# Kernel optimization log

Measured on AMD Instinct MI355X. Metric: run time of the kernel, lower is better.

## Reference

```python
import jax, jax.numpy as jnp
import numpy as np

NUM_ATOMS = 100
D = 32        # initial_atom_dim
H = 16        # hidden_dim (multiplicity per irrep)
NB = 16       # edge_dim / number of bessel basis functions
CUT = 6.0     # radius_cutoff
DEG = 4.0     # degree_norm
OUT = 1       # output_dim
INV4PI = 1.0 / np.sqrt(4.0 * np.pi)  # 'integral' SH normalization


def _bessel(d, nb, cut):
    # e3nn soft_one_hot_linspace(basis='bessel', cutoff=True) * sqrt(nb)
    x = d[:, None]
    n = jnp.arange(1, nb + 1, dtype=d.dtype)
    safe = jnp.maximum(x, 1e-9)
    out = np.sqrt(2.0 / cut) * jnp.sin(n * jnp.pi * x / cut) / safe
    return out * (x < cut) * np.sqrt(float(nb))


def _fc(x, w1, w2):
    # e3nn FullyConnectedNet: fan-in normalized linear layers, silu, no bias
    h = jax.nn.silu(x @ w1 / np.sqrt(x.shape[-1]))
    return h @ w2 / np.sqrt(w1.shape[-1])


def _forward(atomic_numbers, edge_index, coords, atom_emb,
             fc0_w1, fc0_w2, fc1_w1, fc1_w2, w_readout):
    src, dst = edge_index[0], edge_index[1]
    N = coords.shape[0]
    E = src.shape[0]

    vec = coords[src] - coords[dst]                      # [E,3]
    dist = jnp.linalg.norm(vec, axis=-1)                 # [E]
    unit = vec / jnp.maximum(dist, 1e-9)[:, None]

    # spherical harmonics, l=0 and l=1, 'integral' normalization
    y0 = jnp.full((E,), INV4PI, dtype=coords.dtype)      # [E]
    y1 = (np.sqrt(3.0) * INV4PI) * unit                  # [E,3]
    basis = _bessel(dist, NB, CUT)                       # [E,NB]

    x = atom_emb[atomic_numbers]                         # [N,D] (row 0 is padding)

    # ---- layer 0: scalars (D x0e) x (1x0e+1x1o) -> H x0e + H x1o ----
    w = _fc(basis, fc0_w1, fc0_w2)                       # [E, 2*D*H] per-edge TP weights
    wa = w[:, : D * H].reshape(E, D, H)
    wb = w[:, D * H:].reshape(E, D, H)
    xs = x[src]
    n0 = 1.0 / np.sqrt(D)                                # path fan-in norm
    m0 = jnp.einsum('ed,edh->eh', xs, wa) * y0[:, None] * n0          # [E,H]
    m1 = jnp.einsum('ed,edh->eh', xs, wb)[:, :, None] * y1[:, None, :] * n0  # [E,H,3]
    z0 = jax.ops.segment_sum(m0, dst, num_segments=N) / DEG           # [N,H]
    z1 = jax.ops.segment_sum(m1, dst, num_segments=N) / DEG           # [N,H,3]

    # ---- layer 1: (H x0e + H x1o) x (1x0e+1x1o) -> same irreps, skip-connected ----
    w = _fc(basis, fc1_w1, fc1_w2)                       # [E, 4*H*H]
    w1_ = w[:, 0 * H * H:1 * H * H].reshape(E, H, H)     # 0e x 0e -> 0e
    w2_ = w[:, 1 * H * H:2 * H * H].reshape(E, H, H)     # 0e x 1o -> 1o
    w3_ = w[:, 2 * H * H:3 * H * H].reshape(E, H, H)     # 1o x 0e -> 1o
    w4_ = w[:, 3 * H * H:4 * H * H].reshape(E, H, H)     # 1o x 1o -> 0e (CG = dot/sqrt(3))
    s, v = z0[src], z1[src]
    n1 = 1.0 / np.sqrt(2 * H)                            # two paths per output irrep
    dot = jnp.einsum('ehm,em->eh', v, y1) / np.sqrt(3.0)
    o0 = (jnp.einsum('eh,ehk->ek', s, w1_) * y0[:, None]
          + jnp.einsum('eh,ehk->ek', dot, w4_)) * n1
    o1 = (jnp.einsum('eh,ehk->ek', s, w2_)[:, :, None] * y1[:, None, :]
          + jnp.einsum('ehm,ehk->ekm', v, w3_) * y0[:, None, None]) * n1
    z0 = jax.ops.segment_sum(o0, dst, num_segments=N) / DEG + z0      # skip
    z1 = jax.ops.segment_sum(o1, dst, num_segments=N) / DEG + z1

    # ---- scalar readout (o3.Linear onto 0e) + graph sum-pool ----
    node_scalar = z0 @ w_readout / np.sqrt(H)            # [N,OUT]
    return jnp.sum(node_scalar, axis=0)                  # [OUT]


def setup_inputs() -> dict:
    key = jax.random.key(0)
    ks = jax.random.split(key, 9)
    N, E = 10000, 160000
    atomic_numbers = jax.random.randint(ks[0], (N,), 0, NUM_ATOMS)
    coords = jax.random.normal(ks[1], (N, 3), dtype=jnp.float32)
    edge_index = jax.random.randint(ks[2], (2, E), 0, N)
    atom_emb = jax.random.normal(ks[3], (NUM_ATOMS, D), dtype=jnp.float32).at[0].set(0.0)
    fc0_w1 = jax.random.normal(ks[4], (NB, H), dtype=jnp.float32)
    fc0_w2 = jax.random.normal(ks[5], (H, 2 * D * H), dtype=jnp.float32)
    fc1_w1 = jax.random.normal(ks[6], (NB, H), dtype=jnp.float32)
    fc1_w2 = jax.random.normal(ks[7], (H, 4 * H * H), dtype=jnp.float32)
    w_readout = jax.random.normal(ks[8], (H, OUT), dtype=jnp.float32)
    return {"atomic_numbers": atomic_numbers, "coords": coords, "edge_index": edge_index,
            "atom_emb": atom_emb, "fc0_w1": fc0_w1, "fc0_w2": fc0_w2,
            "fc1_w1": fc1_w1, "fc1_w2": fc1_w2, "w_readout": w_readout}


def reference(atomic_numbers, coords, edge_index, atom_emb,
              fc0_w1, fc0_w2, fc1_w1, fc1_w2, w_readout):
    return _forward(atomic_numbers, edge_index, coords, atom_emb,
                    fc0_w1, fc0_w2, fc1_w1, fc1_w2, w_readout)
```

## Files before the change

kernel.cpp:

```cpp
#include <hip/hip_runtime.h>
#include <math.h>


namespace {
constexpr int   NATOMS   = 100;
constexpr int   CAP      = 64;
constexpr float PI_F     = 3.14159265358979323846f;
constexpr float INV4PI_F = 0.28209479177387814f;
constexpr float SQRT3_F  = 1.7320508075688772f;
constexpr float CUT_F    = 6.0f;
constexpr float BASIS_C  = 2.3094010767585034f;
constexpr float N0_F     = 0.17677669529663687f;
constexpr float K0_F = INV4PI_F * N0_F * 0.0625f;
constexpr float K1_F = SQRT3_F * INV4PI_F * N0_F * 0.0625f;
constexpr float P2SC = INV4PI_F * N0_F * (1.0f / 64.0f);
}

__device__ __forceinline__ float silu_fast(float x) {
  return x / (1.0f + __expf(-x));
}

__device__ __forceinline__ float block_reduce_sum(float v) {
  #pragma unroll
  for (int o = 32; o > 0; o >>= 1) v += __shfl_down(v, o, 64);
  __shared__ float ls[8];
  int lane = threadIdx.x & 63;
  int w    = threadIdx.x >> 6;
  if (lane == 0) ls[w] = v;
  __syncthreads();
  float s = 0.f;
  if (threadIdx.x == 0) {
    int nw = (blockDim.x + 63) >> 6;
    for (int i = 0; i < nw; ++i) s += ls[i];
  }
  return s;
}

__global__ void table_kernel(const float* __restrict__ atom_emb,
                             const float* __restrict__ fc0_w2,
                             const float* __restrict__ fc1_w2,
                             const float* __restrict__ w_readout,
                             float* __restrict__ TI,
                             float* __restrict__ G1T, float* __restrict__ G4T,
                             int* __restrict__ dcur,
                             float* __restrict__ out,
                             int N2) {
  int b = blockIdx.x;
  int tt = threadIdx.x;
  if (b < NATOMS) {
    int j = tt >> 4;
    int h = tt & 15;
    float s0 = 0.f, s1 = 0.f;
    #pragma unroll
    for (int d = 0; d < 32; ++d) {
      float x = atom_emb[b * 32 + d];
      s0 = fmaf(x, fc0_w2[j * 1024 + d * 16 + h], s0);
      s1 = fmaf(x, fc0_w2[j * 1024 + 512 + d * 16 + h], s1);
    }
    TI[b * 512 + j * 32 + 2 * h]     = s0;
    TI[b * 512 + j * 32 + 2 * h + 1] = s1;
  } else if (b == NATOMS) {
    int j = tt >> 4;
    int h = tt & 15;
    float g1 = 0.f, g4 = 0.f;
    #pragma unroll
    for (int k = 0; k < 16; ++k) {
      float r = w_readout[k];
      g1 = fmaf(fc1_w2[j * 1024 + h * 16 + k], r, g1);
      g4 = fmaf(fc1_w2[j * 1024 + 768 + h * 16 + k], r, g4);
    }
    G1T[h * 16 + j] = g1;
    G4T[h * 16 + j] = g4;
    if (tt == 0) *out = 0.f;
  } else {
    int idx = (b - NATOMS - 1) * 256 + tt;
    if (idx < N2) dcur[idx] = 0;
  }
}

__global__ void __launch_bounds__(256)
edge_kernel(const int* __restrict__ ei,
            const float* __restrict__ coords,
            const int* __restrict__ an,
            const float* __restrict__ TI,
            const float* __restrict__ fc0_w1,
            const float* __restrict__ fc1_w1,
            int* __restrict__ dcur, int* __restrict__ scur,
            float2* __restrict__ mbuf,
            float4* __restrict__ ubuf,
            float4* __restrict__ sbuf,
            float* __restrict__ hbuf,
            int E) {
  int lane = threadIdx.x & 63;
  int g    = threadIdx.x >> 4;
  int t    = threadIdx.x & 15;
  int base = lane & 48;

  float w0c[16], w1c[16];
  #pragma unroll
  for (int k = 0; k < 16; ++k) {
    w0c[k] = fc0_w1[k * 16 + t];
    w1c[k] = fc1_w1[k * 16 + t];
  }

  const float angc = PI_F / CUT_F;
  int eA = blockIdx.x * 32 + g;
  int eB = eA + 16;
  bool vA = eA < E, vB = eB < E;
  int eAc = vA ? eA : 0, eBc = vB ? eB : 0;

  int sA = ei[eAc], dA = ei[E + eAc];
  int sB = ei[eBc], dB = ei[E + eBc];
  float sxA = coords[3 * sA + 0], syA = coords[3 * sA + 1], szA = coords[3 * sA + 2];
  float dxA = coords[3 * dA + 0], dyA = coords[3 * dA + 1], dzA = coords[3 * dA + 2];
  float sxB = coords[3 * sB + 0], syB = coords[3 * sB + 1], szB = coords[3 * sB + 2];
  float dxB = coords[3 * dB + 0], dyB = coords[3 * dB + 1], dzB = coords[3 * dB + 2];
  int aA = an[sA], aB = an[sB];

  float vxA = sxA - dxA, vyA = syA - dyA, vzA = szA - dzA;
  float vxB = sxB - dxB, vyB = syB - dyB, vzB = szB - dzB;
  float distA = sqrtf(vxA * vxA + vyA * vyA + vzA * vzA);
  float distB = sqrtf(vxB * vxB + vyB * vyB + vzB * vzB);
  float ivA = 1.0f / fmaxf(distA, 1e-9f);
  float ivB = 1.0f / fmaxf(distB, 1e-9f);
  float uxA = vxA * ivA, uyA = vyA * ivA, uzA = vzA * ivA;
  float uxB = vxB * ivB, uyB = vyB * ivB, uzB = vzB * ivB;
  float bcA = (distA < CUT_F) ? (BASIS_C * ivA) : 0.0f;
  float bcB = (distB < CUT_F) ? (BASIS_C * ivB) : 0.0f;

  int dsAv = 0, ssAv = 0, dsBv = 0, ssBv = 0;
  if (t == 0) {
    if (vA) {
      int p = atomicAdd(&dcur[dA], 1), q = atomicAdd(&scur[sA], 1);
      dsAv = dA * CAP + min(p, CAP - 1);
      ssAv = sA * CAP + min(q, CAP - 1);
      ubuf[dsAv] = make_float4(uxA, uyA, uzA, distA);
      sbuf[ssAv] = make_float4(uxA, uyA, uzA, distA);
    }
    if (vB) {
      int p = atomicAdd(&dcur[dB], 1), q = atomicAdd(&scur[sB], 1);
      dsBv = dB * CAP + min(p, CAP - 1);
      ssBv = sB * CAP + min(q, CAP - 1);
      ubuf[dsBv] = make_float4(uxB, uyB, uzB, distB);
      sbuf[ssBv] = make_float4(uxB, uyB, uzB, distB);
    }
  }

  float angA = angc * distA, angB = angc * distB;
  float scA = __sinf(angA), twA = 2.0f * __cosf(angA), spA = 0.f;
  float scB = __sinf(angB), twB = 2.0f * __cosf(angB), spB = 0.f;
  float a0A = 0.f, a1A = 0.f, a0B = 0.f, a1B = 0.f;
  #pragma unroll
  for (int k = 0; k < 16; ++k) {
    a0A = fmaf(scA, w0c[k], a0A);
    a1A = fmaf(scA, w1c[k], a1A);
    a0B = fmaf(scB, w0c[k], a0B);
    a1B = fmaf(scB, w1c[k], a1B);
    float snA = fmaf(twA, scA, -spA); spA = scA; scA = snA;
    float snB = fmaf(twB, scB, -spB); spB = scB; scB = snB;
  }
  float h0A = silu_fast(a0A * bcA * 0.25f);
  float h1A = silu_fast(a1A * bcA * 0.25f);
  float h0B = silu_fast(a0B * bcB * 0.25f);
  float h1B = silu_fast(a1B * bcB * 0.25f);

  int dsA = __shfl(dsAv, base, 64);
  int ssA = __shfl(ssAv, base, 64);
  int dsB = __shfl(dsBv, base, 64);
  int ssB = __shfl(ssBv, base, 64);

  const float2* tpA = (const float2*)(TI + aA * 512) + t;
  const float2* tpB = (const float2*)(TI + aB * 512) + t;
  float u0A = 0.f, u1A = 0.f, u0B = 0.f, u1B = 0.f;
  #pragma unroll
  for (int j = 0; j < 16; ++j) {
    float hjA = __shfl(h0A, base + j, 64);
    float hjB = __shfl(h0B, base + j, 64);
    float2 TA = tpA[j * 16];
    float2 TB = tpB[j * 16];
    u0A = fmaf(hjA, TA.x, u0A);
    u1A = fmaf(hjA, TA.y, u1A);
    u0B = fmaf(hjB, TB.x, u0B);
    u1B = fmaf(hjB, TB.y, u1B);
  }

  if (vA) {
    hbuf[(size_t)ssA * 16 + t] = h1A;
    mbuf[(size_t)dsA * 16 + t] = make_float2(K0_F * u0A, K1_F * u1A);
  }
  if (vB) {
    hbuf[(size_t)ssB * 16 + t] = h1B;
    mbuf[(size_t)dsB * 16 + t] = make_float2(K0_F * u0B, K1_F * u1B);
  }
}

__global__ void __launch_bounds__(256, 4)
node_kernel(const int* __restrict__ dcur,
            const int* __restrict__ scur,
            const float2* __restrict__ mbuf,
            const float4* __restrict__ ubuf,
            const float4* __restrict__ sbuf,
            const float* __restrict__ hbuf,
            const float* __restrict__ G1T,
            const float* __restrict__ G4T,
            const float* __restrict__ w_readout,
            float* __restrict__ out,
            int N) {
  __shared__ float ggs[512];
  ggs[threadIdx.x]       = G1T[threadIdx.x];
  ggs[256 + threadIdx.x] = G4T[threadIdx.x];
  __syncthreads();

  int wave = threadIdx.x >> 6;
  int lane = threadIdx.x & 63;
  int g    = lane >> 4;
  int t    = lane & 15;
  int base = lane & 48;
  int node = blockIdx.x * 4 + wave;
  bool valid = node < N;

  float rr = w_readout[t];
  int cin  = valid ? min(dcur[node], CAP) : 0;
  int cout = valid ? min(scur[node], CAP) : 0;
  size_t nb = (size_t)(valid ? node : 0) * CAP;

  float a0 = 0.f, ax = 0.f, ay = 0.f, az = 0.f;
  for (int i = g; i < cin; i += 4) {
    float2 f  = mbuf[(nb + i) * 16 + t];
    float4 uu = ubuf[nb + i];
    a0 += f.x;
    ax = fmaf(f.y, uu.x, ax);
    ay = fmaf(f.y, uu.y, ay);
    az = fmaf(f.y, uu.z, az);
  }
  a0 += __shfl_xor(a0, 16, 64); a0 += __shfl_xor(a0, 32, 64);
  ax += __shfl_xor(ax, 16, 64); ax += __shfl_xor(ax, 32, 64);
  ay += __shfl_xor(ay, 16, 64); ay += __shfl_xor(ay, 32, 64);
  az += __shfl_xor(az, 16, 64); az += __shfl_xor(az, 32, 64);

  float srcv = (g == 0) ? a0 : ((g == 1) ? ax : (g == 2) ? ay : az);
  int tofs = (g == 0) ? 0 : 256;
  float o = 0.f;
  #pragma unroll
  for (int h = 0; h < 16; ++h) {
    float vh = __shfl(srcv, base + h, 64);
    o = fmaf(ggs[tofs + h * 16 + t], vh, o);
  }
  float Qt  = __shfl(o, t, 64);
  float Pxt = __shfl(o, 16 + t, 64);
  float Pyt = __shfl(o, 32 + t, 64);
  float Pzt = __shfl(o, 48 + t, 64);

  float c = 0.f;
  for (int i = g; i < cout; i += 4) {
    float h1 = hbuf[(nb + i) * 16 + t];
    float4 uu = sbuf[nb + i];
    c = fmaf(h1, fmaf(Pxt, uu.x, fmaf(Pyt, uu.y, fmaf(Pzt, uu.z, Qt))), c);
  }
  c *= P2SC;
  if (valid && g == 0) c = fmaf(a0 * rr, 0.25f, c);
  if (!valid) c = 0.f;

  float tot = block_reduce_sum(c);
  if (threadIdx.x == 0) atomicAdd(out, tot);
}

extern "C" void kernel_launch(void* const* d_in, const int* in_sizes, int n_in,
                              void* d_out, int out_size, void* d_ws, size_t ws_size,
                              hipStream_t stream) {
  const int*   an        = (const int*)d_in[0];
  const float* coords    = (const float*)d_in[1];
  const int*   ei        = (const int*)d_in[2];
  const float* atom_emb  = (const float*)d_in[3];
  const float* fc0_w1    = (const float*)d_in[4];
  const float* fc0_w2    = (const float*)d_in[5];
  const float* fc1_w1    = (const float*)d_in[6];
  const float* fc1_w2    = (const float*)d_in[7];
  const float* w_readout = (const float*)d_in[8];

  int N = in_sizes[0];
  int E = in_sizes[2] / 2;
  size_t slots = (size_t)N * CAP;

  float4* ubuf = (float4*)d_ws;
  float4* sbuf = ubuf + slots;
  float2* mbuf = (float2*)(sbuf + slots);
  float*  hbuf = (float*)(mbuf + slots * 16);
  float*  TI   = hbuf + slots * 16;
  float*  G1T  = TI + NATOMS * 512;
  float*  G4T  = G1T + 256;
  int*    dcur = (int*)(G4T + 256);
  int*    scur = dcur + N;
  float*  out = (float*)d_out;

  int blk = 256;
  int zgrid = (2 * N + blk - 1) / blk;
  table_kernel<<<NATOMS + 1 + zgrid, blk, 0, stream>>>(
      atom_emb, fc0_w2, fc1_w2, w_readout, TI, G1T, G4T, dcur, out, 2 * N);

  edge_kernel<<<(E + 31) / 32, blk, 0, stream>>>(
      ei, coords, an, TI, fc0_w1, fc1_w1, dcur, scur,
      mbuf, ubuf, sbuf, hbuf, E);

  node_kernel<<<(N + 3) / 4, blk, 0, stream>>>(
      dcur, scur, mbuf, ubuf, sbuf, hbuf, G1T, G4T, w_readout, out, N);
}
```

Before: 149.1 us.

## Replace source-bucketed edge buffers with per-node Z table and edge-parallel pass

Removes the second atomic bucketing by source node, along with the sbuf and hbuf slot buffers. The node kernel now writes per-node coefficient vectors (Q, Px, Py, Pz) to zbuf. A new edge-parallel kernel recomputes the layer-1 radial hidden h1 from a compact per-edge unit/dist record and gathers zbuf by source node. This is meant to cut atomics and the large scattered writes of 16 floats per edge, at the cost of an extra kernel launch, per-edge recomputation of the Bessel/MLP, and a random gather.

```diff
diff --git a/kernel.cpp b/kernel.cpp
--- a/kernel.cpp
+++ b/kernel.cpp
@@ -44,7 +44,7 @@
                              float* __restrict__ G1T, float* __restrict__ G4T,
                              int* __restrict__ dcur,
                              float* __restrict__ out,
-                             int N2) {
+                             int N) {
   int b = blockIdx.x;
   int tt = threadIdx.x;
   if (b < NATOMS) {
@@ -74,7 +74,7 @@
     if (tt == 0) *out = 0.f;
   } else {
     int idx = (b - NATOMS - 1) * 256 + tt;
-    if (idx < N2) dcur[idx] = 0;
+    if (idx < N) dcur[idx] = 0;
   }
 }
 
@@ -84,24 +84,19 @@
             const int* __restrict__ an,
             const float* __restrict__ TI,
             const float* __restrict__ fc0_w1,
-            const float* __restrict__ fc1_w1,
-            int* __restrict__ dcur, int* __restrict__ scur,
+            int* __restrict__ dcur,
             float2* __restrict__ mbuf,
             float4* __restrict__ ubuf,
-            float4* __restrict__ sbuf,
-            float* __restrict__ hbuf,
+            float4* __restrict__ evec,
             int E) {
   int lane = threadIdx.x & 63;
   int g    = threadIdx.x >> 4;
   int t    = threadIdx.x & 15;
   int base = lane & 48;
 
-  float w0c[16], w1c[16];
-  #pragma unroll
-  for (int k = 0; k < 16; ++k) {
-    w0c[k] = fc0_w1[k * 16 + t];
-    w1c[k] = fc1_w1[k * 16 + t];
-  }
+  float w0c[16];
+  #pragma unroll
+  for (int k = 0; k < 16; ++k) w0c[k] = fc0_w1[k * 16 + t];
 
   const float angc = PI_F / CUT_F;
   int eA = blockIdx.x * 32 + g;
@@ -128,46 +123,40 @@
   float bcA = (distA < CUT_F) ? (BASIS_C * ivA) : 0.0f;
   float bcB = (distB < CUT_F) ? (BASIS_C * ivB) : 0.0f;
 
-  int dsAv = 0, ssAv = 0, dsBv = 0, ssBv = 0;
+  int dsAv = 0, dsBv = 0;
   if (t == 0) {
     if (vA) {
-      int p = atomicAdd(&dcur[dA], 1), q = atomicAdd(&scur[sA], 1);
+      float4 rec = make_float4(uxA, uyA, uzA, distA);
+      int p = atomicAdd(&dcur[dA], 1);
       dsAv = dA * CAP + min(p, CAP - 1);
-      ssAv = sA * CAP + min(q, CAP - 1);
-      ubuf[dsAv] = make_float4(uxA, uyA, uzA, distA);
-      sbuf[ssAv] = make_float4(uxA, uyA, uzA, distA);
+      ubuf[dsAv] = rec;
+      evec[eA] = rec;
     }
     if (vB) {
-      int p = atomicAdd(&dcur[dB], 1), q = atomicAdd(&scur[sB], 1);
+      float4 rec = make_float4(uxB, uyB, uzB, distB);
+      int p = atomicAdd(&dcur[dB], 1);
       dsBv = dB * CAP + min(p, CAP - 1);
-      ssBv = sB * CAP + min(q, CAP - 1);
-      ubuf[dsBv] = make_float4(uxB, uyB, uzB, distB);
-      sbuf[ssBv] = make_float4(uxB, uyB, uzB, distB);
+      ubuf[dsBv] = rec;
+      evec[eB] = rec;
     }
   }
 
   float angA = angc * distA, angB = angc * distB;
   float scA = __sinf(angA), twA = 2.0f * __cosf(angA), spA = 0.f;
   float scB = __sinf(angB), twB = 2.0f * __cosf(angB), spB = 0.f;
-  float a0A = 0.f, a1A = 0.f, a0B = 0.f, a1B = 0.f;
+  float a0A = 0.f, a0B = 0.f;
   #pragma unroll
   for (int k = 0; k < 16; ++k) {
     a0A = fmaf(scA, w0c[k], a0A);
-    a1A = fmaf(scA, w1c[k], a1A);
     a0B = fmaf(scB, w0c[k], a0B);
-    a1B = fmaf(scB, w1c[k], a1B);
     float snA = fmaf(twA, scA, -spA); spA = scA; scA = snA;
     float snB = fmaf(twB, scB, -spB); spB = scB; scB = snB;
   }
   float h0A = silu_fast(a0A * bcA * 0.25f);
-  float h1A = silu_fast(a1A * bcA * 0.25f);
   float h0B = silu_fast(a0B * bcB * 0.25f);
-  float h1B = silu_fast(a1B * bcB * 0.25f);
 
   int dsA = __shfl(dsAv, base, 64);
-  int ssA = __shfl(ssAv, base, 64);
   int dsB = __shfl(dsBv, base, 64);
-  int ssB = __shfl(ssBv, base, 64);
 
   const float2* tpA = (const float2*)(TI + aA * 512) + t;
   const float2* tpB = (const float2*)(TI + aB * 512) + t;
@@ -184,26 +173,18 @@
     u1B = fmaf(hjB, TB.y, u1B);
   }
 
-  if (vA) {
-    hbuf[(size_t)ssA * 16 + t] = h1A;
-    mbuf[(size_t)dsA * 16 + t] = make_float2(K0_F * u0A, K1_F * u1A);
-  }
-  if (vB) {
-    hbuf[(size_t)ssB * 16 + t] = h1B;
-    mbuf[(size_t)dsB * 16 + t] = make_float2(K0_F * u0B, K1_F * u1B);
-  }
+  if (vA) mbuf[(size_t)dsA * 16 + t] = make_float2(K0_F * u0A, K1_F * u1A);
+  if (vB) mbuf[(size_t)dsB * 16 + t] = make_float2(K0_F * u0B, K1_F * u1B);
 }
 
 __global__ void __launch_bounds__(256, 4)
 node_kernel(const int* __restrict__ dcur,
-            const int* __restrict__ scur,
             const float2* __restrict__ mbuf,
             const float4* __restrict__ ubuf,
-            const float4* __restrict__ sbuf,
-            const float* __restrict__ hbuf,
             const float* __restrict__ G1T,
             const float* __restrict__ G4T,
             const float* __restrict__ w_readout,
+            float* __restrict__ zbuf,
             float* __restrict__ out,
             int N) {
   __shared__ float ggs[512];
@@ -220,8 +201,7 @@
   bool valid = node < N;
 
   float rr = w_readout[t];
-  int cin  = valid ? min(dcur[node], CAP) : 0;
-  int cout = valid ? min(scur[node], CAP) : 0;
+  int cin = valid ? min(dcur[node], CAP) : 0;
   size_t nb = (size_t)(valid ? node : 0) * CAP;
 
   float a0 = 0.f, ax = 0.f, ay = 0.f, az = 0.f;
@@ -246,21 +226,52 @@
     float vh = __shfl(srcv, base + h, 64);
     o = fmaf(ggs[tofs + h * 16 + t], vh, o);
   }
-  float Qt  = __shfl(o, t, 64);
-  float Pxt = __shfl(o, 16 + t, 64);
-  float Pyt = __shfl(o, 32 + t, 64);
-  float Pzt = __shfl(o, 48 + t, 64);
+  if (valid) zbuf[(size_t)node * 64 + t * 4 + g] = o;
+
+  float p = (valid && g == 0) ? a0 * rr : 0.f;
+  float tot = block_reduce_sum(p);
+  if (threadIdx.x == 0) atomicAdd(out, tot * 0.25f);
+}
+
+__global__ void __launch_bounds__(256, 4)
+phase2_kernel(const int* __restrict__ ei,
+              const float4* __restrict__ evec,
+              const float* __restrict__ fc1_w1,
+              const float* __restrict__ zbuf,
+              float* __restrict__ out,
+              int E) {
+  int t = threadIdx.x & 15;
+  float w1c[16];
+  #pragma unroll
+  for (int k = 0; k < 16; ++k) w1c[k] = fc1_w1[k * 16 + t];
+
+  int gid = (blockIdx.x * blockDim.x + threadIdx.x) >> 4;
+  int ngroups = (gridDim.x * blockDim.x) >> 4;
+  const float angc = PI_F / CUT_F;
 
   float c = 0.f;
-  for (int i = g; i < cout; i += 4) {
-    float h1 = hbuf[(nb + i) * 16 + t];
-    float4 uu = sbuf[nb + i];
-    c = fmaf(h1, fmaf(Pxt, uu.x, fmaf(Pyt, uu.y, fmaf(Pzt, uu.z, Qt))), c);
+  for (int e = gid; e < E; e += ngroups) {
+    int s = ei[e];
+    float4 ev = evec[e];
+    float dist = ev.w;
+    float bc = (dist < CUT_F) ? (BASIS_C / fmaxf(dist, 1e-9f)) : 0.0f;
+
+    float ang = angc * dist;
+    float sc = __sinf(ang);
+    float tw = 2.0f * __cosf(ang);
+    float sp = 0.f, acc = 0.f;
+    #pragma unroll
+    for (int k = 0; k < 16; ++k) {
+      acc = fmaf(sc, w1c[k], acc);
+      float sn = fmaf(tw, sc, -sp);
+      sp = sc; sc = sn;
+    }
+    float h1t = silu_fast(acc * bc * 0.25f);
+
+    float4 z = ((const float4*)(zbuf + (size_t)s * 64))[t];
+    c = fmaf(h1t, fmaf(z.y, ev.x, fmaf(z.z, ev.y, fmaf(z.w, ev.z, z.x))), c);
   }
   c *= P2SC;
-  if (valid && g == 0) c = fmaf(a0 * rr, 0.25f, c);
-  if (!valid) c = 0.f;
-
   float tot = block_reduce_sum(c);
   if (threadIdx.x == 0) atomicAdd(out, tot);
 }
@@ -283,25 +294,25 @@
   size_t slots = (size_t)N * CAP;
 
   float4* ubuf = (float4*)d_ws;
-  float4* sbuf = ubuf + slots;
-  float2* mbuf = (float2*)(sbuf + slots);
-  float*  hbuf = (float*)(mbuf + slots * 16);
-  float*  TI   = hbuf + slots * 16;
+  float4* evec = ubuf + slots;
+  float2* mbuf = (float2*)(evec + E);
+  float*  zbuf = (float*)(mbuf + slots * 16);
+  float*  TI   = zbuf + (size_t)N * 64;
   float*  G1T  = TI + NATOMS * 512;
   float*  G4T  = G1T + 256;
   int*    dcur = (int*)(G4T + 256);
-  int*    scur = dcur + N;
   float*  out = (float*)d_out;
 
   int blk = 256;
-  int zgrid = (2 * N + blk - 1) / blk;
+  int zgrid = (N + blk - 1) / blk;
   table_kernel<<<NATOMS + 1 + zgrid, blk, 0, stream>>>(
-      atom_emb, fc0_w2, fc1_w2, w_readout, TI, G1T, G4T, dcur, out, 2 * N);
+      atom_emb, fc0_w2, fc1_w2, w_readout, TI, G1T, G4T, dcur, out, N);
 
   edge_kernel<<<(E + 31) / 32, blk, 0, stream>>>(
-      ei, coords, an, TI, fc0_w1, fc1_w1, dcur, scur,
-      mbuf, ubuf, sbuf, hbuf, E);
+      ei, coords, an, TI, fc0_w1, dcur, mbuf, ubuf, evec, E);
 
   node_kernel<<<(N + 3) / 4, blk, 0, stream>>>(
-      dcur, scur, mbuf, ubuf, sbuf, hbuf, G1T, G4T, w_readout, out, N);
-}
+      dcur, mbuf, ubuf, G1T, G4T, w_readout, zbuf, out, N);
+
+  phase2_kernel<<<2048, blk, 0, stream>>>(ei, evec, fc1_w1, zbuf, out, E);
+}
```

Result: slower. 178.6 us (+19.8%).

## Split edge kernel into per-edge geometry/bucketing pass and compute pass

Applied to the files above, without the earlier changes.

The edge geometry, atomic slot allocation and ubuf/sbuf scatter move into a new geom_kernel that runs one thread per edge. It writes a per-edge record (unit vector, distance) and an aux record (atom type, slot indices). The compute kernel then reads these records instead of doing serialized lane-0 atomics and coordinate gathers inside 16-lane groups. The aim is to remove the lane-0 bottleneck and raise atomic parallelism, at the cost of an extra launch and extra global traffic of 32 bytes per edge written and then read back.

```diff
diff --git a/kernel.cpp b/kernel.cpp
--- a/kernel.cpp
+++ b/kernel.cpp
@@ -79,16 +79,43 @@
 }
 
 __global__ void __launch_bounds__(256)
-edge_kernel(const int* __restrict__ ei,
+geom_kernel(const int* __restrict__ ei,
             const float* __restrict__ coords,
             const int* __restrict__ an,
+            int* __restrict__ dcur, int* __restrict__ scur,
+            float4* __restrict__ ubuf,
+            float4* __restrict__ sbuf,
+            float4* __restrict__ erec,
+            int4* __restrict__ eaux,
+            int E) {
+  int e = blockIdx.x * blockDim.x + threadIdx.x;
+  if (e >= E) return;
+  int s = ei[e];
+  int d = ei[E + e];
+  float vx = coords[3 * s + 0] - coords[3 * d + 0];
+  float vy = coords[3 * s + 1] - coords[3 * d + 1];
+  float vz = coords[3 * s + 2] - coords[3 * d + 2];
+  float dist = sqrtf(vx * vx + vy * vy + vz * vz);
+  float inv  = 1.0f / fmaxf(dist, 1e-9f);
+  float4 rec = make_float4(vx * inv, vy * inv, vz * inv, dist);
+
+  int dp = atomicAdd(&dcur[d], 1);
+  int sp = atomicAdd(&scur[s], 1);
+  int ds = d * CAP + min(dp, CAP - 1);
+  int ss = s * CAP + min(sp, CAP - 1);
+  ubuf[ds] = rec;
+  sbuf[ss] = rec;
+  erec[e] = rec;
+  eaux[e] = make_int4(an[s], ds, ss, 0);
+}
+
+__global__ void __launch_bounds__(256)
+comp_kernel(const float4* __restrict__ erec,
+            const int4* __restrict__ eaux,
             const float* __restrict__ TI,
             const float* __restrict__ fc0_w1,
             const float* __restrict__ fc1_w1,
-            int* __restrict__ dcur, int* __restrict__ scur,
             float2* __restrict__ mbuf,
-            float4* __restrict__ ubuf,
-            float4* __restrict__ sbuf,
             float* __restrict__ hbuf,
             int E) {
   int lane = threadIdx.x & 63;
@@ -109,42 +136,13 @@
   bool vA = eA < E, vB = eB < E;
   int eAc = vA ? eA : 0, eBc = vB ? eB : 0;
 
-  int sA = ei[eAc], dA = ei[E + eAc];
-  int sB = ei[eBc], dB = ei[E + eBc];
-  float sxA = coords[3 * sA + 0], syA = coords[3 * sA + 1], szA = coords[3 * sA + 2];
-  float dxA = coords[3 * dA + 0], dyA = coords[3 * dA + 1], dzA = coords[3 * dA + 2];
-  float sxB = coords[3 * sB + 0], syB = coords[3 * sB + 1], szB = coords[3 * sB + 2];
-  float dxB = coords[3 * dB + 0], dyB = coords[3 * dB + 1], dzB = coords[3 * dB + 2];
-  int aA = an[sA], aB = an[sB];
-
-  float vxA = sxA - dxA, vyA = syA - dyA, vzA = szA - dzA;
-  float vxB = sxB - dxB, vyB = syB - dyB, vzB = szB - dzB;
-  float distA = sqrtf(vxA * vxA + vyA * vyA + vzA * vzA);
-  float distB = sqrtf(vxB * vxB + vyB * vyB + vzB * vzB);
-  float ivA = 1.0f / fmaxf(distA, 1e-9f);
-  float ivB = 1.0f / fmaxf(distB, 1e-9f);
-  float uxA = vxA * ivA, uyA = vyA * ivA, uzA = vzA * ivA;
-  float uxB = vxB * ivB, uyB = vyB * ivB, uzB = vzB * ivB;
-  float bcA = (distA < CUT_F) ? (BASIS_C * ivA) : 0.0f;
-  float bcB = (distB < CUT_F) ? (BASIS_C * ivB) : 0.0f;
-
-  int dsAv = 0, ssAv = 0, dsBv = 0, ssBv = 0;
-  if (t == 0) {
-    if (vA) {
-      int p = atomicAdd(&dcur[dA], 1), q = atomicAdd(&scur[sA], 1);
-      dsAv = dA * CAP + min(p, CAP - 1);
-      ssAv = sA * CAP + min(q, CAP - 1);
-      ubuf[dsAv] = make_float4(uxA, uyA, uzA, distA);
-      sbuf[ssAv] = make_float4(uxA, uyA, uzA, distA);
-    }
-    if (vB) {
-      int p = atomicAdd(&dcur[dB], 1), q = atomicAdd(&scur[sB], 1);
-      dsBv = dB * CAP + min(p, CAP - 1);
-      ssBv = sB * CAP + min(q, CAP - 1);
-      ubuf[dsBv] = make_float4(uxB, uyB, uzB, distB);
-      sbuf[ssBv] = make_float4(uxB, uyB, uzB, distB);
-    }
-  }
+  float4 rA = erec[eAc];
+  float4 rB = erec[eBc];
+  int4   xA = eaux[eAc];
+  int4   xB = eaux[eBc];
+  float distA = rA.w, distB = rB.w;
+  float bcA = (distA < CUT_F) ? (BASIS_C / fmaxf(distA, 1e-9f)) : 0.0f;
+  float bcB = (distB < CUT_F) ? (BASIS_C / fmaxf(distB, 1e-9f)) : 0.0f;
 
   float angA = angc * distA, angB = angc * distB;
   float scA = __sinf(angA), twA = 2.0f * __cosf(angA), spA = 0.f;
@@ -164,13 +162,8 @@
   float h0B = silu_fast(a0B * bcB * 0.25f);
   float h1B = silu_fast(a1B * bcB * 0.25f);
 
-  int dsA = __shfl(dsAv, base, 64);
-  int ssA = __shfl(ssAv, base, 64);
-  int dsB = __shfl(dsBv, base, 64);
-  int ssB = __shfl(ssBv, base, 64);
-
-  const float2* tpA = (const float2*)(TI + aA * 512) + t;
-  const float2* tpB = (const float2*)(TI + aB * 512) + t;
+  const float2* tpA = (const float2*)(TI + xA.x * 512) + t;
+  const float2* tpB = (const float2*)(TI + xB.x * 512) + t;
   float u0A = 0.f, u1A = 0.f, u0B = 0.f, u1B = 0.f;
   #pragma unroll
   for (int j = 0; j < 16; ++j) {
@@ -185,12 +178,12 @@
   }
 
   if (vA) {
-    hbuf[(size_t)ssA * 16 + t] = h1A;
-    mbuf[(size_t)dsA * 16 + t] = make_float2(K0_F * u0A, K1_F * u1A);
+    hbuf[(size_t)xA.z * 16 + t] = h1A;
+    mbuf[(size_t)xA.y * 16 + t] = make_float2(K0_F * u0A, K1_F * u1A);
   }
   if (vB) {
-    hbuf[(size_t)ssB * 16 + t] = h1B;
-    mbuf[(size_t)dsB * 16 + t] = make_float2(K0_F * u0B, K1_F * u1B);
+    hbuf[(size_t)xB.z * 16 + t] = h1B;
+    mbuf[(size_t)xB.y * 16 + t] = make_float2(K0_F * u0B, K1_F * u1B);
   }
 }
 
@@ -284,7 +277,9 @@
 
   float4* ubuf = (float4*)d_ws;
   float4* sbuf = ubuf + slots;
-  float2* mbuf = (float2*)(sbuf + slots);
+  float4* erec = sbuf + slots;
+  int4*   eaux = (int4*)(erec + E);
+  float2* mbuf = (float2*)(eaux + E);
   float*  hbuf = (float*)(mbuf + slots * 16);
   float*  TI   = hbuf + slots * 16;
   float*  G1T  = TI + NATOMS * 512;
@@ -298,9 +293,11 @@
   table_kernel<<<NATOMS + 1 + zgrid, blk, 0, stream>>>(
       atom_emb, fc0_w2, fc1_w2, w_readout, TI, G1T, G4T, dcur, out, 2 * N);
 
-  edge_kernel<<<(E + 31) / 32, blk, 0, stream>>>(
-      ei, coords, an, TI, fc0_w1, fc1_w1, dcur, scur,
-      mbuf, ubuf, sbuf, hbuf, E);
+  geom_kernel<<<(E + blk - 1) / blk, blk, 0, stream>>>(
+      ei, coords, an, dcur, scur, ubuf, sbuf, erec, eaux, E);
+
+  comp_kernel<<<(E + 31) / 32, blk, 0, stream>>>(
+      erec, eaux, TI, fc0_w1, fc1_w1, mbuf, hbuf, E);
 
   node_kernel<<<(N + 3) / 4, blk, 0, stream>>>(
       dcur, scur, mbuf, ubuf, sbuf, hbuf, G1T, G4T, w_readout, out, N);
```

New measurement: 161.1 us. 8.0% more time.
